# Performance work log

Hardware: AMD Instinct MI355X
Metric: run time of the kernel (lower is better)

## Reference

```python
import jax, jax.numpy as jnp
import numpy as np

B, N, C, H, K = 16, 2048, 64, 128, 16
EPS = 1e-5  # torch BatchNorm1d default eps


def _bn(h, g, b, axes):
    # training-mode batch norm: biased variance over all non-channel axes
    m = h.mean(axes, keepdims=True)
    v = h.var(axes, keepdims=True)
    return (h - m) * jax.lax.rsqrt(v + EPS) * g + b


def _edge_conv(x, W1, b1, g1, be1, W2, b2, g2, be2):
    # x: [B, N, C]; dynamic kNN graph in feature space (per graph), includes self
    sq = jnp.sum(x * x, axis=-1)                                   # [B, N]
    d2 = sq[:, :, None] + sq[:, None, :] - 2.0 * jnp.einsum('bnc,bmc->bnm', x, x)
    idx = jax.lax.top_k(-d2, K)[1]                                 # [B, N, K]
    xj = jax.vmap(lambda xb, ib: xb[ib])(x, idx)                   # [B, N, K, C]
    xi = jnp.broadcast_to(x[:, :, None, :], xj.shape)
    h = jnp.concatenate([xi, xj - xi], axis=-1) @ W1 + b1          # [B, N, K, H]
    h = jax.nn.relu(_bn(h, g1, be1, (0, 1, 2)))
    h = h @ W2 + b2
    h = jax.nn.relu(_bn(h, g2, be2, (0, 1, 2)))
    return h.max(axis=2)                                           # max aggregation -> [B, N, H]


def setup_inputs() -> dict:
    key = jax.random.key(0)
    ks = jax.random.split(key, 8)
    inp = {
        'x': jax.random.normal(ks[0], (B * N, C), jnp.float32),
        'batch': jnp.repeat(jnp.arange(B, dtype=jnp.int32), N),
    }
    i = 1
    for pref in ('s', 't'):
        inp[f'{pref}_W1'] = jax.random.normal(ks[i], (2 * C, H), jnp.float32) * 0.05; i += 1
        inp[f'{pref}_b1'] = jnp.zeros((H,), jnp.float32)
        inp[f'{pref}_g1'] = jnp.ones((H,), jnp.float32)
        inp[f'{pref}_be1'] = jnp.zeros((H,), jnp.float32)
        inp[f'{pref}_W2'] = jax.random.normal(ks[i], (H, H), jnp.float32) * 0.05; i += 1
        inp[f'{pref}_b2'] = jnp.zeros((H,), jnp.float32)
        inp[f'{pref}_g2'] = jnp.ones((H,), jnp.float32)
        inp[f'{pref}_be2'] = jnp.zeros((H,), jnp.float32)
    inp['f_W'] = jax.random.normal(ks[i], (2 * H, H), jnp.float32) * 0.05
    inp['f_b'] = jnp.zeros((H,), jnp.float32)
    inp['f_g'] = jnp.ones((H,), jnp.float32)
    inp['f_be'] = jnp.zeros((H,), jnp.float32)
    return inp


def reference(x, batch,
              s_W1, s_b1, s_g1, s_be1, s_W2, s_b2, s_g2, s_be2,
              t_W1, t_b1, t_g1, t_be1, t_W2, t_b2, t_g2, t_be2,
              f_W, f_b, f_g, f_be):
    # batch is sorted with B equal-size graphs of N nodes -> reshape
    xb = x.reshape(B, N, C)
    xs = _edge_conv(xb, s_W1, s_b1, s_g1, s_be1, s_W2, s_b2, s_g2, s_be2)
    xt = _edge_conv(xb, t_W1, t_b1, t_g1, t_be1, t_W2, t_b2, t_g2, t_be2)
    comb = jnp.concatenate([xs, xt], axis=-1).reshape(B * N, 2 * H)
    h = comb @ f_W + f_b
    return jax.nn.relu(_bn(h, f_g, f_be, (0,)))
```

## Files before the change

### kernel.cpp

```cpp
#include <hip/hip_runtime.h>
#include <hip/hip_bf16.h>
#include <stdint.h>

#define NB 16
#define NN 2048
#define NC 64
#define NH 128
#define NK 16
#define NS (NB*NN)
#define NSK (NS*NK)
#define EPSV 1e-5f

typedef __attribute__((ext_vector_type(8))) short short8;
typedef __attribute__((ext_vector_type(8))) _Float16 half8;
typedef __attribute__((ext_vector_type(8))) unsigned short ushort8;
typedef __attribute__((ext_vector_type(4))) float f32x4;

__device__ __forceinline__ unsigned short f2bf(float x) {
  union { float f; unsigned u; } v; v.f = x;
  unsigned r = v.u + 0x7fffu + ((v.u >> 16) & 1u);
  return (unsigned short)(r >> 16);
}

__device__ __forceinline__ unsigned orderf(float f) {
  unsigned u = __float_as_uint(f);
  return u ^ ((unsigned)((int)u >> 31) | 0x80000000u);
}

__device__ __forceinline__ unsigned long long shfl_xor_u64(unsigned long long v, int m) {
  unsigned lo = (unsigned)(v & 0xffffffffull);
  unsigned hi = (unsigned)(v >> 32);
  lo = __shfl_xor(lo, m, 64);
  hi = __shfl_xor(hi, m, 64);
  return (((unsigned long long)hi) << 32) | lo;
}

__global__ void prep_x(const float* __restrict__ x, float* __restrict__ sq,
                       unsigned short* __restrict__ xh, unsigned short* __restrict__ xl) {
  int i = blockIdx.x * blockDim.x + threadIdx.x;
  if (i >= NS) return;
  const float4* x4 = (const float4*)(x + (size_t)i * NC);
  float s = 0.f;
#pragma unroll
  for (int k = 0; k < 8; k++) {
    float4 a = x4[2*k], b = x4[2*k+1];
    float f[8] = {a.x,a.y,a.z,a.w,b.x,b.y,b.z,b.w};
    ushort8 hv, lv;
#pragma unroll
    for (int j = 0; j < 8; j++) {
      float v = f[j];
      s += v*v;
      _Float16 h = (_Float16)v;
      float r = v - (float)h;
      _Float16 l = (_Float16)r;
      union { _Float16 ff; unsigned short u; } ch, cl;
      ch.ff = h; cl.ff = l;
      hv[j] = ch.u; lv[j] = cl.u;
    }
    *(ushort8*)(xh + (size_t)i*64 + k*8) = hv;
    *(ushort8*)(xl + (size_t)i*64 + k*8) = lv;
  }
  sq[i] = s;
}

__global__ __launch_bounds__(256) void knn3_kernel(const unsigned short* __restrict__ xh,
                                                   const unsigned short* __restrict__ xl,
                                                   const float* __restrict__ sq,
                                                   int* __restrict__ nbr) {
  __shared__ unsigned short rAh[64*64], rAl[64*64];
  __shared__ unsigned short cBh[64*64], cBl[64*64];
  __shared__ float gram[64*68];
  __shared__ float sqc[64];
  int b = blockIdx.x >> 5;
  int rb = blockIdx.x & 31;
  int w = threadIdx.x >> 6, lane = threadIdx.x & 63;
  int n16 = lane & 15, q = lane >> 4;
  int rowbase = b*NN + rb*64;

  {
    int r = threadIdx.x >> 2;
    int c0 = (threadIdx.x & 3) * 2;
#pragma unroll
    for (int cc = 0; cc < 2; cc++) {
      int c = c0 + cc;
      int pos = (c ^ (r & 7)) * 8;
      *(ushort8*)&rAh[r*64 + pos] = *(const ushort8*)(xh + (size_t)(rowbase + r)*64 + c*8);
      *(ushort8*)&rAl[r*64 + pos] = *(const ushort8*)(xl + (size_t)(rowbase + r)*64 + c*8);
    }
  }
  __syncthreads();
  half8 ah[2], al[2];
  int m = w*16 + n16;
#pragma unroll
  for (int ks = 0; ks < 2; ks++) {
    int pos = ((ks*4 + q) ^ (m & 7)) * 8;
    ah[ks] = *(const half8*)&rAh[m*64 + pos];
    al[ks] = *(const half8*)&rAl[m*64 + pos];
  }
  float sqr = sq[rowbase + m];

  unsigned long long keys[16];
#pragma unroll
  for (int i = 0; i < 16; i++) keys[i] = ~0ull;
  unsigned whi = 0xffffffffu;

  for (int ch = 0; ch < 32; ch++) {
    int colbase = b*NN + ch*64;
    __syncthreads();
    {
      int r = threadIdx.x >> 2;
      int c0 = (threadIdx.x & 3) * 2;
#pragma unroll
      for (int cc = 0; cc < 2; cc++) {
        int c = c0 + cc;
        int pos = (c ^ (r & 7)) * 8;
        *(ushort8*)&cBh[r*64 + pos] = *(const ushort8*)(xh + (size_t)(colbase + r)*64 + c*8);
        *(ushort8*)&cBl[r*64 + pos] = *(const ushort8*)(xl + (size_t)(colbase + r)*64 + c*8);
      }
      if (threadIdx.x < 64) sqc[threadIdx.x] = sq[colbase + threadIdx.x];
    }
    __syncthreads();
    f32x4 acc[4];
#pragma unroll
    for (int ci = 0; ci < 4; ci++) acc[ci] = (f32x4){0.f,0.f,0.f,0.f};
#pragma unroll
    for (int ks = 0; ks < 2; ks++) {
#pragma unroll
      for (int ci = 0; ci < 4; ci++) {
        int n = ci*16 + n16;
        int pos = ((ks*4 + q) ^ (n & 7)) * 8;
        half8 bh = *(const half8*)&cBh[n*64 + pos];
        half8 bl = *(const half8*)&cBl[n*64 + pos];
        acc[ci] = __builtin_amdgcn_mfma_f32_16x16x32_f16(ah[ks], bh, acc[ci], 0, 0, 0);
        acc[ci] = __builtin_amdgcn_mfma_f32_16x16x32_f16(al[ks], bh, acc[ci], 0, 0, 0);
        acc[ci] = __builtin_amdgcn_mfma_f32_16x16x32_f16(ah[ks], bl, acc[ci], 0, 0, 0);
      }
    }
#pragma unroll
    for (int ci = 0; ci < 4; ci++)
#pragma unroll
      for (int r = 0; r < 4; r++)
        gram[(w*16 + q*4 + r)*68 + ci*16 + n16] = acc[ci][r];
    __syncthreads();
    const float* gp = &gram[(size_t)(w*16 + n16)*68 + q*16];
    const float* sc = &sqc[q*16];
    unsigned mask = 0;
#pragma unroll
    for (int i4 = 0; i4 < 4; i4++) {
      float4 g4 = *(const float4*)(gp + i4*4);
      float4 s4 = *(const float4*)(sc + i4*4);
      float d0 = fmaf(-2.f, g4.x, sqr + s4.x);
      float d1 = fmaf(-2.f, g4.y, sqr + s4.y);
      float d2 = fmaf(-2.f, g4.z, sqr + s4.z);
      float d3 = fmaf(-2.f, g4.w, sqr + s4.w);
      if (orderf(d0) <= whi) mask |= 1u << (i4*4+0);
      if (orderf(d1) <= whi) mask |= 1u << (i4*4+1);
      if (orderf(d2) <= whi) mask |= 1u << (i4*4+2);
      if (orderf(d3) <= whi) mask |= 1u << (i4*4+3);
    }
    while (mask) {
      int i = __builtin_ctz(mask);
      mask &= mask - 1;
      float g = gp[i];
      float dd = fmaf(-2.f, g, sqr + sc[i]);
      unsigned long long key = ((unsigned long long)orderf(dd) << 32) |
                               (unsigned)(colbase + q*16 + i);
#pragma unroll
      for (int j = 0; j < 16; j++) {
        bool cl = key < keys[j];
        unsigned long long lo = cl ? key : keys[j];
        key = cl ? keys[j] : key;
        keys[j] = lo;
      }
      whi = (unsigned)(keys[15] >> 32);
    }
  }
  for (int j = 0; j < NK; j++) {
    unsigned long long mk = keys[0];
#pragma unroll
    for (int i = 1; i < 16; i++) mk = (keys[i] < mk) ? keys[i] : mk;
    unsigned long long o = shfl_xor_u64(mk, 16); mk = (o < mk) ? o : mk;
    o = shfl_xor_u64(mk, 32); mk = (o < mk) ? o : mk;
#pragma unroll
    for (int i = 0; i < 16; i++) if (keys[i] == mk) keys[i] = ~0ull;
    if (q == 0) nbr[(size_t)(rowbase + m)*NK + j] = (int)(mk & 0xffffffffu);
  }
}

__global__ void prep_weights(const float* __restrict__ sW1, const float* __restrict__ sW2,
                             const float* __restrict__ tW1, const float* __restrict__ tW2,
                             const float* __restrict__ fW,
                             unsigned short* __restrict__ sW1t, unsigned short* __restrict__ sW2t,
                             unsigned short* __restrict__ tW1t, unsigned short* __restrict__ tW2t,
                             unsigned short* __restrict__ fWt) {
  int i = blockIdx.x * blockDim.x + threadIdx.x;
  if (i < 4*16384) {
    int mi = i >> 14, e = i & 16383;
    int h = e >> 7, k = e & 127;
    const float* src = (mi==0) ? sW1 : (mi==1) ? sW2 : (mi==2) ? tW1 : tW2;
    unsigned short* dst = (mi==0) ? sW1t : (mi==1) ? sW2t : (mi==2) ? tW1t : tW2t;
    dst[h*128 + k] = f2bf(src[k*128 + h]);
  } else {
    int e = i - 4*16384;
    if (e < 128*256) {
      int h = e >> 8, k = e & 255;
      fWt[h*256 + k] = f2bf(fW[k*128 + h]);
    }
  }
}

__global__ __launch_bounds__(256) void pnode_kernel(
    const float* __restrict__ x,
    const unsigned short* __restrict__ sW1t, const unsigned short* __restrict__ tW1t,
    float* __restrict__ PS, float* __restrict__ PT) {
  __shared__ unsigned short xt_[64*64];
  int rowbase = blockIdx.x * 64;
  int lane = threadIdx.x & 63;
  int wave = threadIdx.x >> 6;
  int n16 = lane & 15, q = lane >> 4;
  int cb = wave * 32;
  {
    int r = threadIdx.x >> 2, part = threadIdx.x & 3;
    const float4* xp = (const float4*)(x + (size_t)(rowbase + r) * NC) + part*4;
#pragma unroll
    for (int cc = 0; cc < 2; cc++) {
      int c = part*2 + cc;
      float4 a = xp[cc*2], b = xp[cc*2+1];
      int pos = (c ^ (r & 7)) * 8;
      unsigned short* d = &xt_[r*64 + pos];
      d[0]=f2bf(a.x); d[1]=f2bf(a.y); d[2]=f2bf(a.z); d[3]=f2bf(a.w);
      d[4]=f2bf(b.x); d[5]=f2bf(b.y); d[6]=f2bf(b.z); d[7]=f2bf(b.w);
    }
  }
  __syncthreads();
  f32x4 aS[4][2], aT[4][2];
#pragma unroll
  for (int ri = 0; ri < 4; ri++)
#pragma unroll
    for (int ci = 0; ci < 2; ci++) {
      aS[ri][ci] = (f32x4){0.f,0.f,0.f,0.f};
      aT[ri][ci] = (f32x4){0.f,0.f,0.f,0.f};
    }
#pragma unroll
  for (int ks = 0; ks < 2; ks++) {
    short8 af[4];
#pragma unroll
    for (int ri = 0; ri < 4; ri++) {
      int m = ri*16 + n16;
      af[ri] = *(const short8*)&xt_[m*64 + (((ks*4+q) ^ (m & 7)))*8];
    }
#pragma unroll
    for (int ci = 0; ci < 2; ci++) {
      int col = cb + ci*16 + n16;
      short8 bS = *(const short8*)(sW1t + col*128 + (ks*4+q)*8);
      short8 bT = *(const short8*)(tW1t + col*128 + (ks*4+q)*8);
#pragma unroll
      for (int ri = 0; ri < 4; ri++) {
        aS[ri][ci] = __builtin_amdgcn_mfma_f32_16x16x32_bf16(af[ri], bS, aS[ri][ci], 0, 0, 0);
        aT[ri][ci] = __builtin_amdgcn_mfma_f32_16x16x32_bf16(af[ri], bT, aT[ri][ci], 0, 0, 0);
      }
    }
  }
#pragma unroll
  for (int ri = 0; ri < 4; ri++)
#pragma unroll
    for (int ci = 0; ci < 2; ci++) {
      int col = cb + ci*16 + n16;
#pragma unroll
      for (int r = 0; r < 4; r++) {
        int row = rowbase + ri*16 + q*4 + r;
        PS[(size_t)row*128 + col] = aS[ri][ci][r];
        PT[(size_t)row*128 + col] = aT[ri][ci][r];
      }
    }
}

__global__ __launch_bounds__(256) void dbuild_kernel(
    const float* __restrict__ x, const int* __restrict__ nbr,
    unsigned short* __restrict__ D) {
  int g = blockIdx.x & 15, chunk = blockIdx.x >> 4;
  int r4 = threadIdx.x >> 2, part = threadIdx.x & 3;
#pragma unroll
  for (int it = 0; it < 8; it++) {
    int s = g*32768 + chunk*512 + it*64 + r4;
    int node = s >> 4;
    int ng = nbr[s];
    const float4* xi = (const float4*)(x + (size_t)node * NC) + part*4;
    const float4* xj = (const float4*)(x + (size_t)ng  * NC) + part*4;
    unsigned short* dst = D + ((size_t)(s >> 6)) * 4096 + (size_t)(s & 63) * 64;
#pragma unroll
    for (int cc = 0; cc < 2; cc++) {
      int c = part*2 + cc;
      float4 a0 = xi[cc*2], a1 = xi[cc*2+1];
      float4 b0 = xj[cc*2], b1 = xj[cc*2+1];
      int pos = (c ^ (s & 7)) * 8;
      unsigned short* d = dst + pos;
      d[0]=f2bf(b0.x-a0.x); d[1]=f2bf(b0.y-a0.y); d[2]=f2bf(b0.z-a0.z); d[3]=f2bf(b0.w-a0.w);
      d[4]=f2bf(b1.x-a1.x); d[5]=f2bf(b1.y-a1.y); d[6]=f2bf(b1.z-a1.z); d[7]=f2bf(b1.w-a1.w);
    }
  }
}

template<int MODE>
__global__ __launch_bounds__(256, 2) void mlp_pass2(
    const unsigned short* __restrict__ D,
    const float* __restrict__ PS, const float* __restrict__ PT,
    const unsigned short* __restrict__ sW1t, const unsigned short* __restrict__ sW2t,
    const unsigned short* __restrict__ tW1t, const unsigned short* __restrict__ tW2t,
    const float* __restrict__ affS1, const float* __restrict__ affS2,
    const float* __restrict__ affT1, const float* __restrict__ affT2,
    float* __restrict__ statS, float* __restrict__ statT,
    float* __restrict__ xoutS, float* __restrict__ xoutT) {
  __shared__ unsigned short dlds[64*64];
  __shared__ unsigned short atile[(MODE >= 1) ? 64*128 : 64];
  int wave = threadIdx.x >> 6;
  int lane = threadIdx.x & 63;
  int n16 = lane & 15, q = lane >> 4;
  int cb = wave * 32;

  float s1S[2], h1S[2], s2S[2], h2S[2];
  float s1T[2], h1T[2], s2T[2], h2T[2];
  if (MODE >= 1) {
#pragma unroll
    for (int ci = 0; ci < 2; ci++) {
      int col = cb + ci*16 + n16;
      s1S[ci] = affS1[col]; h1S[ci] = affS1[128 + col];
      s1T[ci] = affT1[col]; h1T[ci] = affT1[128 + col];
    }
  }
  if (MODE == 2) {
#pragma unroll
    for (int ci = 0; ci < 2; ci++) {
      int col = cb + ci*16 + n16;
      s2S[ci] = affS2[col]; h2S[ci] = affS2[128 + col];
      s2T[ci] = affT2[col]; h2T[ci] = affT2[128 + col];
    }
  }
  float psS[2] = {0,0}, ps2S[2] = {0,0};
  float psT[2] = {0,0}, ps2T[2] = {0,0};

  for (int it = 0; it < 4; it++) {
    int tile = blockIdx.x*4 + it;
    __syncthreads();
    {
      const ushort8* src = (const ushort8*)(D + (size_t)tile*4096);
      ushort8* dst = (ushort8*)dlds;
      dst[threadIdx.x] = src[threadIdx.x];
      dst[threadIdx.x + 256] = src[threadIdx.x + 256];
    }
    __syncthreads();
    int node0 = tile*4;
    float pS[4][2], pT[4][2];
#pragma unroll
    for (int ri = 0; ri < 4; ri++)
#pragma unroll
      for (int ci = 0; ci < 2; ci++) {
        int col = cb + ci*16 + n16;
        pS[ri][ci] = PS[(size_t)(node0+ri)*128 + col];
        pT[ri][ci] = PT[(size_t)(node0+ri)*128 + col];
      }

#pragma unroll
    for (int st = 0; st < 2; st++) {
      const unsigned short* W1t = st ? tW1t : sW1t;
      const unsigned short* W2t = st ? tW2t : sW2t;
      const float* sc1 = st ? s1T : s1S;  const float* sh1 = st ? h1T : h1S;
      const float* sc2 = st ? s2T : s2S;  const float* sh2 = st ? h2T : h2S;
      float (*pp)[2] = st ? pT : pS;
      float* ps  = st ? psT : psS;
      float* ps2 = st ? ps2T : ps2S;
      float* xout = st ? xoutT : xoutS;

      f32x4 acc[4][2];
#pragma unroll
      for (int ri = 0; ri < 4; ri++)
#pragma unroll
        for (int ci = 0; ci < 2; ci++)
          acc[ri][ci] = (f32x4){0.f,0.f,0.f,0.f};
#pragma unroll
      for (int ks = 0; ks < 2; ks++) {
        short8 af[4], bf[2];
#pragma unroll
        for (int ri = 0; ri < 4; ri++) {
          int m = ri*16 + n16;
          af[ri] = *(const short8*)&dlds[m*64 + ((ks*4+q) ^ (m & 7))*8];
        }
#pragma unroll
        for (int ci = 0; ci < 2; ci++) {
          int col = cb + ci*16 + n16;
          bf[ci] = *(const short8*)(W1t + col*128 + 64 + (ks*4+q)*8);
        }
#pragma unroll
        for (int ri = 0; ri < 4; ri++)
#pragma unroll
          for (int ci = 0; ci < 2; ci++)
            acc[ri][ci] = __builtin_amdgcn_mfma_f32_16x16x32_bf16(af[ri], bf[ci], acc[ri][ci], 0, 0, 0);
      }
      if (MODE == 0) {
#pragma unroll
        for (int ci = 0; ci < 2; ci++)
#pragma unroll
          for (int ri = 0; ri < 4; ri++)
#pragma unroll
            for (int r = 0; r < 4; r++) {
              float v = acc[ri][ci][r] + pp[ri][ci];
              ps[ci] += v; ps2[ci] += v*v;
            }
        continue;
      }
#pragma unroll
      for (int ri = 0; ri < 4; ri++)
#pragma unroll
        for (int ci = 0; ci < 2; ci++) {
          int colL = cb + ci*16 + n16;
          int kc8 = colL >> 3;
#pragma unroll
          for (int r = 0; r < 4; r++) {
            float v = acc[ri][ci][r] + pp[ri][ci];
            v = fmaxf(v * sc1[ci] + sh1[ci], 0.f);
            int rowL = ri*16 + q*4 + r;
            int pos = ((kc8 ^ (rowL & 7)) << 3) + (colL & 7);
            atile[rowL*128 + pos] = f2bf(v);
          }
        }
      __syncthreads();
      f32x4 acc2[4][2];
#pragma unroll
      for (int ri = 0; ri < 4; ri++)
#pragma unroll
        for (int ci = 0; ci < 2; ci++)
          acc2[ri][ci] = (f32x4){0.f,0.f,0.f,0.f};
#pragma unroll
      for (int ks = 0; ks < 4; ks++) {
        short8 a2[4], bf[2];
#pragma unroll
        for (int ri = 0; ri < 4; ri++) {
          int mm = ri*16 + n16;
          int kc8 = (ks*4 + q) ^ (mm & 7);
          a2[ri] = *(const short8*)&atile[mm*128 + kc8*8];
        }
#pragma unroll
        for (int ci = 0; ci < 2; ci++) {
          int col = cb + ci*16 + n16;
          bf[ci] = *(const short8*)(W2t + col*128 + ks*32 + q*8);
        }
#pragma unroll
        for (int ri = 0; ri < 4; ri++)
#pragma unroll
          for (int ci = 0; ci < 2; ci++)
            acc2[ri][ci] = __builtin_amdgcn_mfma_f32_16x16x32_bf16(a2[ri], bf[ci], acc2[ri][ci], 0, 0, 0);
      }
      if (MODE == 1) {
#pragma unroll
        for (int ci = 0; ci < 2; ci++)
#pragma unroll
          for (int ri = 0; ri < 4; ri++)
#pragma unroll
            for (int r = 0; r < 4; r++) {
              float v = acc2[ri][ci][r];
              ps[ci] += v; ps2[ci] += v*v;
            }
      } else {
#pragma unroll
        for (int ri = 0; ri < 4; ri++)
#pragma unroll
          for (int ci = 0; ci < 2; ci++) {
            int col = cb + ci*16 + n16;
            float vm = 0.f;
#pragma unroll
            for (int r = 0; r < 4; r++) {
              float v = fmaxf(acc2[ri][ci][r] * sc2[ci] + sh2[ci], 0.f);
              vm = fmaxf(vm, v);
            }
            vm = fmaxf(vm, __shfl_xor(vm, 16, 64));
            vm = fmaxf(vm, __shfl_xor(vm, 32, 64));
            if (q == 0) xout[(size_t)(node0 + ri)*128 + col] = vm;
          }
      }
      if (st == 0) __syncthreads();
    }
  }
  if (MODE <= 1) {
#pragma unroll
    for (int ci = 0; ci < 2; ci++) {
      int col = cb + ci*16 + n16;
      float a = psS[ci], a2 = ps2S[ci], b = psT[ci], b2 = ps2T[ci];
      a  += __shfl_xor(a, 16, 64);  a  += __shfl_xor(a, 32, 64);
      a2 += __shfl_xor(a2, 16, 64); a2 += __shfl_xor(a2, 32, 64);
      b  += __shfl_xor(b, 16, 64);  b  += __shfl_xor(b, 32, 64);
      b2 += __shfl_xor(b2, 16, 64); b2 += __shfl_xor(b2, 32, 64);
      if (q == 0) {
        atomicAdd(&statS[col], a);
        atomicAdd(&statS[128 + col], a2);
        atomicAdd(&statT[col], b);
        atomicAdd(&statT[128 + col], b2);
      }
    }
  }
}

__global__ void finalize_kernel(const float* __restrict__ stats,
                                const float* __restrict__ g,
                                const float* __restrict__ be,
                                float* __restrict__ aff, float invcount) {
  int c = threadIdx.x;
  if (c < 128) {
    float mean = stats[c] * invcount;
    float var = stats[128 + c] * invcount - mean*mean;
    float scale = g[c] / sqrtf(var + EPSV);
    aff[c] = scale;
    aff[128 + c] = be[c] - mean * scale;
  }
}

__global__ __launch_bounds__(128) void final_pass(
    const float* __restrict__ xs,
    const float* __restrict__ xt,
    const unsigned short* __restrict__ fWt,
    float* __restrict__ gout,
    float* __restrict__ stats) {
  __shared__ unsigned short tile[64 * 256];
  int wave = threadIdx.x >> 6, lane = threadIdx.x & 63;
  int n16 = lane & 15, q = lane >> 4;
  int cb = wave * 64;
  int s0 = blockIdx.x * 64;
  {
    int r = threadIdx.x >> 1, half = threadIdx.x & 1;
    const float4* src = (const float4*)((half ? xt : xs) + (size_t)(s0 + r) * 128);
#pragma unroll
    for (int kk = 0; kk < 32; kk++) {
      float4 v = src[kk];
      int kc8 = half*16 + (kk >> 1);
      int pos = ((kc8 ^ (r & 7)) << 3) + ((kk & 1) << 2);
      unsigned short* d = &tile[r*256 + pos];
      d[0]=f2bf(v.x); d[1]=f2bf(v.y); d[2]=f2bf(v.z); d[3]=f2bf(v.w);
    }
  }
  __syncthreads();
  f32x4 acc[4][4];
#pragma unroll
  for (int ri = 0; ri < 4; ri++)
#pragma unroll
    for (int ci = 0; ci < 4; ci++)
      acc[ri][ci] = (f32x4){0.f,0.f,0.f,0.f};
#pragma unroll
  for (int ks = 0; ks < 8; ks++) {
    short8 af[4], bf[4];
#pragma unroll
    for (int ri = 0; ri < 4; ri++) {
      int mm = ri*16 + n16;
      int kc8 = (ks*4 + q) ^ (mm & 7);
      af[ri] = *(const short8*)&tile[mm*256 + kc8*8];
    }
#pragma unroll
    for (int ci = 0; ci < 4; ci++) {
      int col = cb + ci*16 + n16;
      bf[ci] = *(const short8*)(fWt + col*256 + ks*32 + q*8);
    }
#pragma unroll
    for (int ri = 0; ri < 4; ri++)
#pragma unroll
      for (int ci = 0; ci < 4; ci++)
        acc[ri][ci] = __builtin_amdgcn_mfma_f32_16x16x32_bf16(af[ri], bf[ci], acc[ri][ci], 0, 0, 0);
  }
  float ps[4] = {0,0,0,0}, ps2[4] = {0,0,0,0};
#pragma unroll
  for (int ri = 0; ri < 4; ri++)
#pragma unroll
    for (int ci = 0; ci < 4; ci++) {
      int col = cb + ci*16 + n16;
#pragma unroll
      for (int r = 0; r < 4; r++) {
        float v = acc[ri][ci][r];
        int row = s0 + ri*16 + q*4 + r;
        gout[(size_t)row*128 + col] = v;
        ps[ci] += v; ps2[ci] += v*v;
      }
    }
#pragma unroll
  for (int ci = 0; ci < 4; ci++) {
    float s = ps[ci], s2 = ps2[ci];
    s  += __shfl_xor(s, 16, 64);  s  += __shfl_xor(s, 32, 64);
    s2 += __shfl_xor(s2, 16, 64); s2 += __shfl_xor(s2, 32, 64);
    if (q == 0) {
      int col = cb + ci*16 + n16;
      atomicAdd(&stats[col], s);
      atomicAdd(&stats[128 + col], s2);
    }
  }
}

__global__ void apply_bn_kernel(float* __restrict__ out, const float* __restrict__ aff) {
  int i = blockIdx.x * blockDim.x + threadIdx.x;
  if (i < NS*NH) {
    int c = i & 127;
    out[i] = fmaxf(out[i] * aff[c] + aff[128 + c], 0.f);
  }
}

extern "C" void kernel_launch(void* const* d_in, const int* in_sizes, int n_in,
                              void* d_out, int out_size, void* d_ws, size_t ws_size,
                              hipStream_t stream) {
  const float* x   = (const float*)d_in[0];
  const float* sW1 = (const float*)d_in[2];
  const float* sg1 = (const float*)d_in[4];
  const float* sbe1= (const float*)d_in[5];
  const float* sW2 = (const float*)d_in[6];
  const float* sg2 = (const float*)d_in[8];
  const float* sbe2= (const float*)d_in[9];
  const float* tW1 = (const float*)d_in[10];
  const float* tg1 = (const float*)d_in[12];
  const float* tbe1= (const float*)d_in[13];
  const float* tW2 = (const float*)d_in[14];
  const float* tg2 = (const float*)d_in[16];
  const float* tbe2= (const float*)d_in[17];
  const float* fW  = (const float*)d_in[18];
  const float* fg  = (const float*)d_in[20];
  const float* fbe = (const float*)d_in[21];
  float* out = (float*)d_out;

  char* w = (char*)d_ws;
  float* sq = (float*)w;                 w += (size_t)NS*4;
  int* nbr = (int*)w;                    w += (size_t)NSK*4;
  unsigned short* sW1t = (unsigned short*)w; w += 32768;
  unsigned short* sW2t = (unsigned short*)w; w += 32768;
  unsigned short* tW1t = (unsigned short*)w; w += 32768;
  unsigned short* tW2t = (unsigned short*)w; w += 32768;
  unsigned short* fWt  = (unsigned short*)w; w += 65536;
  float* stats = (float*)w;              w += 2560*4;
  float* xs = (float*)w;                 w += (size_t)NS*NH*4;
  float* xt = (float*)w;                 w += (size_t)NS*NH*4;
  unsigned short* xh = (unsigned short*)w; w += (size_t)NS*64*2;
  unsigned short* xl = (unsigned short*)w; w += (size_t)NS*64*2;
  unsigned short* Dg = (unsigned short*)w; w += (size_t)NSK*64*2;
  float* PS = (float*)w;                 w += (size_t)NS*128*4;
  float* PT = (float*)w;                 w += (size_t)NS*128*4;

  float* st_s1 = stats;        float* af_s1 = stats + 256;
  float* st_s2 = stats + 512;  float* af_s2 = stats + 768;
  float* st_t1 = stats + 1024; float* af_t1 = stats + 1280;
  float* st_t2 = stats + 1536; float* af_t2 = stats + 1792;
  float* st_f  = stats + 2048; float* af_f  = stats + 2304;

  hipMemsetAsync(stats, 0, 2560*4, stream);
  prep_weights<<<(4*16384 + 128*256 + 255)/256, 256, 0, stream>>>(
      sW1, sW2, tW1, tW2, fW, sW1t, sW2t, tW1t, tW2t, fWt);
  prep_x<<<NS/256, 256, 0, stream>>>(x, sq, xh, xl);
  knn3_kernel<<<NB*32, 256, 0, stream>>>(xh, xl, sq, nbr);
  pnode_kernel<<<NS/64, 256, 0, stream>>>(x, sW1t, tW1t, PS, PT);
  dbuild_kernel<<<1024, 256, 0, stream>>>(x, nbr, Dg);

  const float inv1 = 1.f/(float)NSK, invf = 1.f/(float)NS;
  mlp_pass2<0><<<2048,256,0,stream>>>(Dg, PS, PT, sW1t, sW2t, tW1t, tW2t,
      nullptr, nullptr, nullptr, nullptr, st_s1, st_t1, nullptr, nullptr);
  finalize_kernel<<<1,128,0,stream>>>(st_s1, sg1, sbe1, af_s1, inv1);
  finalize_kernel<<<1,128,0,stream>>>(st_t1, tg1, tbe1, af_t1, inv1);
  mlp_pass2<1><<<2048,256,0,stream>>>(Dg, PS, PT, sW1t, sW2t, tW1t, tW2t,
      af_s1, nullptr, af_t1, nullptr, st_s2, st_t2, nullptr, nullptr);
  finalize_kernel<<<1,128,0,stream>>>(st_s2, sg2, sbe2, af_s2, inv1);
  finalize_kernel<<<1,128,0,stream>>>(st_t2, tg2, tbe2, af_t2, inv1);
  mlp_pass2<2><<<2048,256,0,stream>>>(Dg, PS, PT, sW1t, sW2t, tW1t, tW2t,
      af_s1, af_s2, af_t1, af_t2, nullptr, nullptr, xs, xt);
  final_pass<<<NS/64, 128, 0, stream>>>(xs, xt, fWt, out, st_f);
  finalize_kernel<<<1,128,0,stream>>>(st_f, fg, fbe, af_f, invf);
  apply_bn_kernel<<<(NS*NH)/256, 256, 0, stream>>>(out, af_f);
}
```

Measured before the change: 588.9 us.

## Fuse D-build with layer-1 stats pass; swap kNN MFMA operands to drop gram LDS

The kNN kernel swaps the MFMA operand order so each lane's accumulator holds distances for its own row. Distances are then filtered straight from registers, which removes the gram shared-memory round trip and one barrier per chunk. The edge-difference build kernel is merged with the MODE 0 statistics pass: each tile of D is written to global memory and also staged in LDS, then used immediately for the first-layer MFMA and the BN1 sum and sum-of-squares. This drops a separate kernel launch and one full re-read of D, at the cost of a heavier fused kernel and a fixed-unrolled insertion loop in kNN that may diverge.

```diff
diff --git a/kernel.cpp b/kernel.cpp
--- a/kernel.cpp
+++ b/kernel.cpp
@@ -63,13 +63,12 @@
   sq[i] = s;
 }
 
-__global__ __launch_bounds__(256) void knn3_kernel(const unsigned short* __restrict__ xh,
+__global__ __launch_bounds__(256) void knn4_kernel(const unsigned short* __restrict__ xh,
                                                    const unsigned short* __restrict__ xl,
                                                    const float* __restrict__ sq,
                                                    int* __restrict__ nbr) {
   __shared__ unsigned short rAh[64*64], rAl[64*64];
   __shared__ unsigned short cBh[64*64], cBl[64*64];
-  __shared__ float gram[64*68];
   __shared__ float sqc[64];
   int b = blockIdx.x >> 5;
   int rb = blockIdx.x & 31;
@@ -89,20 +88,20 @@
     }
   }
   __syncthreads();
-  half8 ah[2], al[2];
+  half8 bh[2], bl[2];
   int m = w*16 + n16;
 #pragma unroll
   for (int ks = 0; ks < 2; ks++) {
     int pos = ((ks*4 + q) ^ (m & 7)) * 8;
-    ah[ks] = *(const half8*)&rAh[m*64 + pos];
-    al[ks] = *(const half8*)&rAl[m*64 + pos];
+    bh[ks] = *(const half8*)&rAh[m*64 + pos];
+    bl[ks] = *(const half8*)&rAl[m*64 + pos];
   }
   float sqr = sq[rowbase + m];
 
   unsigned long long keys[16];
 #pragma unroll
   for (int i = 0; i < 16; i++) keys[i] = ~0ull;
-  unsigned whi = 0xffffffffu;
+  float wd2 = __builtin_inff();
 
   for (int ch = 0; ch < 32; ch++) {
     int colbase = b*NN + ch*64;
@@ -129,51 +128,41 @@
       for (int ci = 0; ci < 4; ci++) {
         int n = ci*16 + n16;
         int pos = ((ks*4 + q) ^ (n & 7)) * 8;
-        half8 bh = *(const half8*)&cBh[n*64 + pos];
-        half8 bl = *(const half8*)&cBl[n*64 + pos];
-        acc[ci] = __builtin_amdgcn_mfma_f32_16x16x32_f16(ah[ks], bh, acc[ci], 0, 0, 0);
-        acc[ci] = __builtin_amdgcn_mfma_f32_16x16x32_f16(al[ks], bh, acc[ci], 0, 0, 0);
-        acc[ci] = __builtin_amdgcn_mfma_f32_16x16x32_f16(ah[ks], bl, acc[ci], 0, 0, 0);
-      }
-    }
+        half8 ah_ = *(const half8*)&cBh[n*64 + pos];
+        half8 al_ = *(const half8*)&cBl[n*64 + pos];
+        acc[ci] = __builtin_amdgcn_mfma_f32_16x16x32_f16(ah_, bh[ks], acc[ci], 0, 0, 0);
+        acc[ci] = __builtin_amdgcn_mfma_f32_16x16x32_f16(al_, bh[ks], acc[ci], 0, 0, 0);
+        acc[ci] = __builtin_amdgcn_mfma_f32_16x16x32_f16(ah_, bl[ks], acc[ci], 0, 0, 0);
+      }
+    }
+    float d2v[16];
+    unsigned mask = 0;
 #pragma unroll
     for (int ci = 0; ci < 4; ci++)
 #pragma unroll
-      for (int r = 0; r < 4; r++)
-        gram[(w*16 + q*4 + r)*68 + ci*16 + n16] = acc[ci][r];
-    __syncthreads();
-    const float* gp = &gram[(size_t)(w*16 + n16)*68 + q*16];
-    const float* sc = &sqc[q*16];
-    unsigned mask = 0;
-#pragma unroll
-    for (int i4 = 0; i4 < 4; i4++) {
-      float4 g4 = *(const float4*)(gp + i4*4);
-      float4 s4 = *(const float4*)(sc + i4*4);
-      float d0 = fmaf(-2.f, g4.x, sqr + s4.x);
-      float d1 = fmaf(-2.f, g4.y, sqr + s4.y);
-      float d2 = fmaf(-2.f, g4.z, sqr + s4.z);
-      float d3 = fmaf(-2.f, g4.w, sqr + s4.w);
-      if (orderf(d0) <= whi) mask |= 1u << (i4*4+0);
-      if (orderf(d1) <= whi) mask |= 1u << (i4*4+1);
-      if (orderf(d2) <= whi) mask |= 1u << (i4*4+2);
-      if (orderf(d3) <= whi) mask |= 1u << (i4*4+3);
-    }
-    while (mask) {
-      int i = __builtin_ctz(mask);
-      mask &= mask - 1;
-      float g = gp[i];
-      float dd = fmaf(-2.f, g, sqr + sc[i]);
-      unsigned long long key = ((unsigned long long)orderf(dd) << 32) |
-                               (unsigned)(colbase + q*16 + i);
-#pragma unroll
-      for (int j = 0; j < 16; j++) {
-        bool cl = key < keys[j];
-        unsigned long long lo = cl ? key : keys[j];
-        key = cl ? keys[j] : key;
-        keys[j] = lo;
-      }
-      whi = (unsigned)(keys[15] >> 32);
-    }
+      for (int r = 0; r < 4; r++) {
+        int idx = ci*4 + r;
+        float d2 = fmaf(-2.f, acc[ci][r], sqr + sqc[ci*16 + q*4 + r]);
+        d2v[idx] = d2;
+        mask |= (d2 <= wd2) ? (1u << idx) : 0u;
+      }
+#pragma unroll
+    for (int i = 0; i < 16; i++) {
+      if (mask & (1u << i)) {
+        int col = colbase + (i >> 2)*16 + q*4 + (i & 3);
+        unsigned long long key = ((unsigned long long)orderf(d2v[i]) << 32) | (unsigned)col;
+#pragma unroll
+        for (int j = 0; j < 16; j++) {
+          bool cl = key < keys[j];
+          unsigned long long lo = cl ? key : keys[j];
+          key = cl ? keys[j] : key;
+          keys[j] = lo;
+        }
+      }
+    }
+    unsigned whi = (unsigned)(keys[15] >> 32);
+    wd2 = (whi == 0xffffffffu) ? __builtin_inff()
+        : __uint_as_float((whi & 0x80000000u) ? (whi ^ 0x80000000u) : ~whi);
   }
   for (int j = 0; j < NK; j++) {
     unsigned long long mk = keys[0];
@@ -275,28 +264,107 @@
     }
 }
 
-__global__ __launch_bounds__(256) void dbuild_kernel(
+__global__ __launch_bounds__(256, 2) void dstat_kernel(
     const float* __restrict__ x, const int* __restrict__ nbr,
-    unsigned short* __restrict__ D) {
-  int g = blockIdx.x & 15, chunk = blockIdx.x >> 4;
-  int r4 = threadIdx.x >> 2, part = threadIdx.x & 3;
-#pragma unroll
-  for (int it = 0; it < 8; it++) {
-    int s = g*32768 + chunk*512 + it*64 + r4;
-    int node = s >> 4;
-    int ng = nbr[s];
-    const float4* xi = (const float4*)(x + (size_t)node * NC) + part*4;
-    const float4* xj = (const float4*)(x + (size_t)ng  * NC) + part*4;
-    unsigned short* dst = D + ((size_t)(s >> 6)) * 4096 + (size_t)(s & 63) * 64;
-#pragma unroll
-    for (int cc = 0; cc < 2; cc++) {
-      int c = part*2 + cc;
-      float4 a0 = xi[cc*2], a1 = xi[cc*2+1];
-      float4 b0 = xj[cc*2], b1 = xj[cc*2+1];
-      int pos = (c ^ (s & 7)) * 8;
-      unsigned short* d = dst + pos;
-      d[0]=f2bf(b0.x-a0.x); d[1]=f2bf(b0.y-a0.y); d[2]=f2bf(b0.z-a0.z); d[3]=f2bf(b0.w-a0.w);
-      d[4]=f2bf(b1.x-a1.x); d[5]=f2bf(b1.y-a1.y); d[6]=f2bf(b1.z-a1.z); d[7]=f2bf(b1.w-a1.w);
+    const unsigned short* __restrict__ sW1t, const unsigned short* __restrict__ tW1t,
+    const float* __restrict__ PS, const float* __restrict__ PT,
+    unsigned short* __restrict__ D,
+    float* __restrict__ statS, float* __restrict__ statT) {
+  __shared__ unsigned short dlds[64*64];
+  int wave = threadIdx.x >> 6, lane = threadIdx.x & 63;
+  int n16 = lane & 15, q = lane >> 4;
+  int cb = wave * 32;
+  int g = blockIdx.x & 15, sub = blockIdx.x >> 4;
+  float psS[2]={0,0}, ps2S[2]={0,0}, psT[2]={0,0}, ps2T[2]={0,0};
+
+  for (int it = 0; it < 4; it++) {
+    int tile = g*512 + sub*4 + it;
+    __syncthreads();
+    {
+      int r4 = threadIdx.x >> 2, part = threadIdx.x & 3;
+      int s = tile*64 + r4;
+      int node = s >> 4;
+      int ng = nbr[s];
+      const float4* xi = (const float4*)(x + (size_t)node * NC) + part*4;
+      const float4* xj = (const float4*)(x + (size_t)ng  * NC) + part*4;
+      unsigned short* dstg = D + (size_t)tile*4096 + (size_t)r4*64;
+#pragma unroll
+      for (int cc = 0; cc < 2; cc++) {
+        int c = part*2 + cc;
+        float4 a0 = xi[cc*2], a1 = xi[cc*2+1];
+        float4 b0 = xj[cc*2], b1 = xj[cc*2+1];
+        int pos = (c ^ (r4 & 7)) * 8;
+        ushort8 dv;
+        dv[0]=f2bf(b0.x-a0.x); dv[1]=f2bf(b0.y-a0.y); dv[2]=f2bf(b0.z-a0.z); dv[3]=f2bf(b0.w-a0.w);
+        dv[4]=f2bf(b1.x-a1.x); dv[5]=f2bf(b1.y-a1.y); dv[6]=f2bf(b1.z-a1.z); dv[7]=f2bf(b1.w-a1.w);
+        *(ushort8*)(dstg + pos) = dv;
+        *(ushort8*)(dlds + r4*64 + pos) = dv;
+      }
+    }
+    __syncthreads();
+    int node0 = tile*4;
+    float pS[4][2], pT[4][2];
+#pragma unroll
+    for (int ri = 0; ri < 4; ri++)
+#pragma unroll
+      for (int ci = 0; ci < 2; ci++) {
+        int col = cb + ci*16 + n16;
+        pS[ri][ci] = PS[(size_t)(node0+ri)*128 + col];
+        pT[ri][ci] = PT[(size_t)(node0+ri)*128 + col];
+      }
+    f32x4 aS[4][2], aT[4][2];
+#pragma unroll
+    for (int ri = 0; ri < 4; ri++)
+#pragma unroll
+      for (int ci = 0; ci < 2; ci++) {
+        aS[ri][ci] = (f32x4){0.f,0.f,0.f,0.f};
+        aT[ri][ci] = (f32x4){0.f,0.f,0.f,0.f};
+      }
+#pragma unroll
+    for (int ks = 0; ks < 2; ks++) {
+      short8 af[4];
+#pragma unroll
+      for (int ri = 0; ri < 4; ri++) {
+        int m = ri*16 + n16;
+        af[ri] = *(const short8*)&dlds[m*64 + ((ks*4+q) ^ (m & 7))*8];
+      }
+#pragma unroll
+      for (int ci = 0; ci < 2; ci++) {
+        int col = cb + ci*16 + n16;
+        short8 bS = *(const short8*)(sW1t + col*128 + 64 + (ks*4+q)*8);
+        short8 bT = *(const short8*)(tW1t + col*128 + 64 + (ks*4+q)*8);
+#pragma unroll
+        for (int ri = 0; ri < 4; ri++) {
+          aS[ri][ci] = __builtin_amdgcn_mfma_f32_16x16x32_bf16(af[ri], bS, aS[ri][ci], 0, 0, 0);
+          aT[ri][ci] = __builtin_amdgcn_mfma_f32_16x16x32_bf16(af[ri], bT, aT[ri][ci], 0, 0, 0);
+        }
+      }
+    }
+#pragma unroll
+    for (int ci = 0; ci < 2; ci++)
+#pragma unroll
+      for (int ri = 0; ri < 4; ri++)
+#pragma unroll
+        for (int r = 0; r < 4; r++) {
+          float vS = aS[ri][ci][r] + pS[ri][ci];
+          float vT = aT[ri][ci][r] + pT[ri][ci];
+          psS[ci] += vS; ps2S[ci] += vS*vS;
+          psT[ci] += vT; ps2T[ci] += vT*vT;
+        }
+  }
+#pragma unroll
+  for (int ci = 0; ci < 2; ci++) {
+    int col = cb + ci*16 + n16;
+    float a = psS[ci], a2 = ps2S[ci], b2v = psT[ci], b3 = ps2T[ci];
+    a   += __shfl_xor(a, 16, 64);   a   += __shfl_xor(a, 32, 64);
+    a2  += __shfl_xor(a2, 16, 64);  a2  += __shfl_xor(a2, 32, 64);
+    b2v += __shfl_xor(b2v, 16, 64); b2v += __shfl_xor(b2v, 32, 64);
+    b3  += __shfl_xor(b3, 16, 64);  b3  += __shfl_xor(b3, 32, 64);
+    if (q == 0) {
+      atomicAdd(&statS[col], a);
+      atomicAdd(&statS[128 + col], a2);
+      atomicAdd(&statT[col], b2v);
+      atomicAdd(&statT[128 + col], b3);
     }
   }
 }
@@ -312,7 +380,7 @@
     float* __restrict__ statS, float* __restrict__ statT,
     float* __restrict__ xoutS, float* __restrict__ xoutT) {
   __shared__ unsigned short dlds[64*64];
-  __shared__ unsigned short atile[(MODE >= 1) ? 64*128 : 64];
+  __shared__ unsigned short atile[64*128];
   int wave = threadIdx.x >> 6;
   int lane = threadIdx.x & 63;
   int n16 = lane & 15, q = lane >> 4;
@@ -320,13 +388,11 @@
 
   float s1S[2], h1S[2], s2S[2], h2S[2];
   float s1T[2], h1T[2], s2T[2], h2T[2];
-  if (MODE >= 1) {
-#pragma unroll
-    for (int ci = 0; ci < 2; ci++) {
-      int col = cb + ci*16 + n16;
-      s1S[ci] = affS1[col]; h1S[ci] = affS1[128 + col];
-      s1T[ci] = affT1[col]; h1T[ci] = affT1[128 + col];
-    }
+#pragma unroll
+  for (int ci = 0; ci < 2; ci++) {
+    int col = cb + ci*16 + n16;
+    s1S[ci] = affS1[col]; h1S[ci] = affS1[128 + col];
+    s1T[ci] = affT1[col]; h1T[ci] = affT1[128 + col];
   }
   if (MODE == 2) {
 #pragma unroll
@@ -395,18 +461,6 @@
 #pragma unroll
           for (int ci = 0; ci < 2; ci++)
             acc[ri][ci] = __builtin_amdgcn_mfma_f32_16x16x32_bf16(af[ri], bf[ci], acc[ri][ci], 0, 0, 0);
-      }
-      if (MODE == 0) {
-#pragma unroll
-        for (int ci = 0; ci < 2; ci++)
-#pragma unroll
-          for (int ri = 0; ri < 4; ri++)
-#pragma unroll
-            for (int r = 0; r < 4; r++) {
-              float v = acc[ri][ci][r] + pp[ri][ci];
-              ps[ci] += v; ps2[ci] += v*v;
-            }
-        continue;
       }
 #pragma unroll
       for (int ri = 0; ri < 4; ri++)
@@ -480,7 +534,7 @@
       if (st == 0) __syncthreads();
     }
   }
-  if (MODE <= 1) {
+  if (MODE == 1) {
 #pragma unroll
     for (int ci = 0; ci < 2; ci++) {
       int col = cb + ci*16 + n16;
@@ -646,13 +700,11 @@
   prep_weights<<<(4*16384 + 128*256 + 255)/256, 256, 0, stream>>>(
       sW1, sW2, tW1, tW2, fW, sW1t, sW2t, tW1t, tW2t, fWt);
   prep_x<<<NS/256, 256, 0, stream>>>(x, sq, xh, xl);
-  knn3_kernel<<<NB*32, 256, 0, stream>>>(xh, xl, sq, nbr);
+  knn4_kernel<<<NB*32, 256, 0, stream>>>(xh, xl, sq, nbr);
   pnode_kernel<<<NS/64, 256, 0, stream>>>(x, sW1t, tW1t, PS, PT);
-  dbuild_kernel<<<1024, 256, 0, stream>>>(x, nbr, Dg);
+  dstat_kernel<<<2048, 256, 0, stream>>>(x, nbr, sW1t, tW1t, PS, PT, Dg, st_s1, st_t1);
 
   const float inv1 = 1.f/(float)NSK, invf = 1.f/(float)NS;
-  mlp_pass2<0><<<2048,256,0,stream>>>(Dg, PS, PT, sW1t, sW2t, tW1t, tW2t,
-      nullptr, nullptr, nullptr, nullptr, st_s1, st_t1, nullptr, nullptr);
   finalize_kernel<<<1,128,0,stream>>>(st_s1, sg1, sbe1, af_s1, inv1);
   finalize_kernel<<<1,128,0,stream>>>(st_t1, tg1, tbe1, af_t1, inv1);
   mlp_pass2<1><<<2048,256,0,stream>>>(Dg, PS, PT, sW1t, sW2t, tW1t, tW2t,
```

Measured after the change: 703.5 us. 1.19x slower.
